# Optimization experiments

Measured on AMD Instinct MI355X. Metric: run time of the kernel, lower is better.

Reference implementation:

```python
import jax, jax.numpy as jnp
import numpy as np

DIM = 2048
NUM_HEADS = 16
HEAD_DIM = DIM // NUM_HEADS  # 128
LC = HEAD_DIM // 2           # 64 complex pairs per head
B, S = 2, 2048
EPS = 1e-6


def setup_inputs() -> dict:
    key = jax.random.key(0)
    ks = jax.random.split(key, 12)
    x = jax.random.normal(ks[0], (B, S, DIM), dtype=jnp.float32)
    # freqs: unit-modulus complex rotations stored as (cos, sin), shape [S,1,LC,2]
    theta = jax.random.uniform(ks[1], (S, 1, LC), dtype=jnp.float32) * (2.0 * np.pi)
    freqs = jnp.stack([jnp.cos(theta), jnp.sin(theta)], axis=-1)
    scale = 0.02
    wq = jax.random.normal(ks[2], (DIM, DIM), dtype=jnp.float32) * scale
    bq = jnp.zeros((DIM,), dtype=jnp.float32)
    wk = jax.random.normal(ks[3], (DIM, DIM), dtype=jnp.float32) * scale
    bk = jnp.zeros((DIM,), dtype=jnp.float32)
    wv = jax.random.normal(ks[4], (DIM, DIM), dtype=jnp.float32) * scale
    bv = jnp.zeros((DIM,), dtype=jnp.float32)
    wo = jax.random.normal(ks[5], (DIM, DIM), dtype=jnp.float32) * scale
    bo = jnp.zeros((DIM,), dtype=jnp.float32)
    gq = jnp.ones((DIM,), dtype=jnp.float32)   # RMSNorm weight for q
    gk = jnp.ones((DIM,), dtype=jnp.float32)   # RMSNorm weight for k
    return {"x": x, "freqs": freqs, "wq": wq, "bq": bq, "wk": wk, "bk": bk,
            "wv": wv, "bv": bv, "wo": wo, "bo": bo, "gq": gq, "gk": gk}


def _rms_norm(x, g):
    xf = x.astype(jnp.float32)
    y = xf * jax.lax.rsqrt(jnp.mean(xf * xf, axis=-1, keepdims=True) + EPS)
    return y.astype(x.dtype) * g


def _rope_apply(x, freqs):
    # x: [B,S,D] -> complex pairs [B,S,H,LC,2]; freqs: [S,1,LC,2] (cos,sin)
    b, s, _ = x.shape
    xp = x.astype(jnp.float32).reshape(b, s, NUM_HEADS, LC, 2)
    xr, xi = xp[..., 0], xp[..., 1]
    cr = freqs[None, :, :, :, 0]  # [1,S,1,LC]
    ci = freqs[None, :, :, :, 1]
    out_r = xr * cr - xi * ci
    out_i = xr * ci + xi * cr
    out = jnp.stack([out_r, out_i], axis=-1).reshape(b, s, DIM)
    return out.astype(x.dtype)


def _attention(q, k, v):
    # q,k,v: [B,S,D] -> multihead SDPA -> [B,S,D]
    b, s, _ = q.shape
    qh = q.reshape(b, s, NUM_HEADS, HEAD_DIM).transpose(0, 2, 1, 3)
    kh = k.reshape(b, s, NUM_HEADS, HEAD_DIM).transpose(0, 2, 1, 3)
    vh = v.reshape(b, s, NUM_HEADS, HEAD_DIM).transpose(0, 2, 1, 3)
    scale = 1.0 / np.sqrt(HEAD_DIM).astype(np.float32)
    scores = jnp.einsum('bhqd,bhkd->bhqk', qh, kh) * scale
    probs = jax.nn.softmax(scores, axis=-1)
    out = jnp.einsum('bhqk,bhkd->bhqd', probs, vh)
    return out.transpose(0, 2, 1, 3).reshape(b, s, DIM)


def reference(x, freqs, wq, bq, wk, bk, wv, bv, wo, bo, gq, gk):
    q = _rms_norm(x @ wq.T + bq, gq)
    k = _rms_norm(x @ wk.T + bk, gk)
    v = x @ wv.T + bv
    q = _rope_apply(q, freqs)
    k = _rope_apply(k, freqs)
    attn = _attention(q, k, v)
    return attn @ wo.T + bo
```

## Files before the change

kernel.cpp:

```cpp
#include <hip/hip_runtime.h>
#include <cstdint>

typedef __bf16 bf16;
typedef __bf16 bf16x8 __attribute__((ext_vector_type(8)));
typedef __bf16 bf16x4 __attribute__((ext_vector_type(4)));
typedef float f32x4 __attribute__((ext_vector_type(4)));

#define DIMN 2048
#define SEQ  2048
#define NH   16
#define HD   128

__device__ __forceinline__ void gld_lds16(const bf16* g, bf16* l) {
    __builtin_amdgcn_global_load_lds(
        (const __attribute__((address_space(1))) void*)g,
        (__attribute__((address_space(3))) void*)l,
        16, 0, 0);
}

__global__ __launch_bounds__(256) void cast_all(
    const float* __restrict__ x,
    const float* __restrict__ wq, const float* __restrict__ wk,
    const float* __restrict__ wv, const float* __restrict__ wo,
    bf16* __restrict__ xb,
    bf16* __restrict__ wqb, bf16* __restrict__ wkb,
    bf16* __restrict__ wvb, bf16* __restrict__ wob)
{
    int id = blockIdx.x;
    const float* src; bf16* dst; int i;
    if (id < 8192) { src = x; dst = xb; i = id * 256 + threadIdx.x; }
    else {
        id -= 8192;
        int w = id >> 12; id &= 4095;
        src = (w == 0) ? wq : (w == 1) ? wk : (w == 2) ? wv : wo;
        dst = (w == 0) ? wqb : (w == 1) ? wkb : (w == 2) ? wvb : wob;
        i = id * 256 + threadIdx.x;
    }
    float4 v = ((const float4*)src)[i];
    bf16x4 o;
    o[0] = (bf16)v.x; o[1] = (bf16)v.y; o[2] = (bf16)v.z; o[3] = (bf16)v.w;
    ((bf16x4*)dst)[i] = o;
}

template<int OUT_F32>
__global__ __launch_bounds__(256) void gemm_bt(
    const bf16* __restrict__ A,
    const bf16* __restrict__ Bw0, const bf16* __restrict__ Bw1, const bf16* __restrict__ Bw2,
    const float* __restrict__ bias0, const float* __restrict__ bias1, const float* __restrict__ bias2,
    void* __restrict__ C0, void* __restrict__ C1, void* __restrict__ C2)
{
    const int K = DIMN, N = DIMN;
    const int vtm = (!OUT_F32) && (blockIdx.z == 2);
    const bf16* Ap; const bf16* Bp; const float* bias; void* Cout;
    if (blockIdx.z == 0)      { Ap = A;   Bp = Bw0; bias = bias0; Cout = C0; }
    else if (blockIdx.z == 1) { Ap = A;   Bp = Bw1; bias = bias1; Cout = C1; }
    else                      { Ap = Bw2; Bp = A;   bias = bias2; Cout = C2; }

    __shared__ __attribute__((aligned(16))) bf16 As[128 * 64];
    __shared__ __attribute__((aligned(16))) bf16 Bs[128 * 64];

    const int t    = threadIdx.x;
    const int lane = t & 63, wave = t >> 6;
    const int l15  = lane & 15, quad = lane >> 4;
    const int wm   = (wave >> 1) * 64, wn = (wave & 1) * 64;
    const long bm = vtm ? (long)blockIdx.x * 128 : (long)blockIdx.y * 128;
    const long bn = vtm ? (long)blockIdx.y * 128 : (long)blockIdx.x * 128;

    const bf16* agp[4]; const bf16* bgp[4]; bf16* asd[4]; bf16* bsd[4];
#pragma unroll
    for (int it = 0; it < 4; it++) {
        int fs  = it * 256 + t;
        int row = fs >> 3;
        int gs  = (fs & 7) ^ (row & 7);
        agp[it] = Ap + (bm + row) * (long)K + gs * 8;
        bgp[it] = Bp + (bn + row) * (long)K + gs * 8;
        asd[it] = As + fs * 8;
        bsd[it] = Bs + fs * 8;
    }
    const int swl = l15 & 7;

    f32x4 acc[4][4] = {};

    for (int k0 = 0; k0 < K; k0 += 64) {
#pragma unroll
        for (int it = 0; it < 4; it++) {
            gld_lds16(agp[it] + k0, asd[it]);
            gld_lds16(bgp[it] + k0, bsd[it]);
        }
        __syncthreads();

#pragma unroll
        for (int ks2 = 0; ks2 < 2; ks2++) {
            const int sw = ((ks2 * 4 + quad) ^ swl) * 8;
            bf16x8 af[4], bfr[4];
#pragma unroll
            for (int i = 0; i < 4; i++)
                af[i] = *(const bf16x8*)(As + (wm + i * 16 + l15) * 64 + sw);
#pragma unroll
            for (int j = 0; j < 4; j++)
                bfr[j] = *(const bf16x8*)(Bs + (wn + j * 16 + l15) * 64 + sw);
#pragma unroll
            for (int i = 0; i < 4; i++)
#pragma unroll
                for (int j = 0; j < 4; j++)
                    acc[i][j] = __builtin_amdgcn_mfma_f32_16x16x32_bf16(af[i], bfr[j], acc[i][j], 0, 0, 0);
        }
        __syncthreads();
    }

    if (vtm) {
#pragma unroll
        for (int j = 0; j < 4; j++) {
            const long col = bn + wn + j * 16 + l15;
            const long cb = col >> 11, cs = col & (SEQ - 1);
#pragma unroll
            for (int i = 0; i < 4; i++) {
                const long m0 = bm + wm + i * 16 + quad * 4;
#pragma unroll
                for (int r = 0; r < 4; r++)
                    ((bf16*)Cout)[((cb * DIMN + m0 + r) * SEQ) + cs] =
                        (bf16)(acc[i][j][r] + bias[m0 + r]);
            }
        }
    } else {
#pragma unroll
        for (int j = 0; j < 4; j++) {
            const long col = bn + wn + j * 16 + l15;
            const float bv = bias[col];
#pragma unroll
            for (int i = 0; i < 4; i++) {
                const long row0 = bm + wm + i * 16 + quad * 4;
#pragma unroll
                for (int r = 0; r < 4; r++) {
                    float v = acc[i][j][r] + bv;
                    if (OUT_F32) ((float*)Cout)[(row0 + r) * N + col] = v;
                    else         ((bf16*)Cout)[(row0 + r) * N + col] = (bf16)v;
                }
            }
        }
    }
}

__global__ __launch_bounds__(256) void norm_prep(
    bf16* __restrict__ q, bf16* __restrict__ k,
    const float* __restrict__ gq, const float* __restrict__ gk,
    const float* __restrict__ freqs)
{
    const int id = blockIdx.x;
    const int t = threadIdx.x;
    const int qk  = id >> 12;
    const int row = id & 4095;
    bf16* ptr = qk ? k : q;
    const float* g = qk ? gk : gq;
    const float osc = qk ? 1.0f : 0.12753138080219222f;
    const int s = row & (SEQ - 1);
    const int lane = t & 63, wave = t >> 6;

    bf16* base = ptr + (long)row * DIMN + t * 8;
    bf16x8 raw = *(const bf16x8*)base;
    float v[8]; float ss = 0.f;
#pragma unroll
    for (int j = 0; j < 8; j++) { v[j] = (float)raw[j]; ss += v[j] * v[j]; }
#pragma unroll
    for (int off = 32; off; off >>= 1) ss += __shfl_xor(ss, off, 64);
    __shared__ float red[4];
    if (lane == 0) red[wave] = ss;
    __syncthreads();
    float tot = red[0] + red[1] + red[2] + red[3];
    float rn = rsqrtf(tot * (1.0f / DIMN) + 1e-6f);

    const int e0 = t * 8;
    bf16x8 o;
#pragma unroll
    for (int pp = 0; pp < 4; pp++) {
        int e = e0 + pp * 2;
        float xr = v[pp * 2]     * rn * g[e];
        float xi = v[pp * 2 + 1] * rn * g[e + 1];
        int lc = (e >> 1) & 63;
        float cr = freqs[s * 128 + lc * 2];
        float ci = freqs[s * 128 + lc * 2 + 1];
        o[pp * 2]     = (bf16)((xr * cr - xi * ci) * osc);
        o[pp * 2 + 1] = (bf16)((xr * ci + xi * cr) * osc);
    }
    *(bf16x8*)base = o;
}

__global__ __launch_bounds__(512, 2) void attention(
    const bf16* __restrict__ Q, const bf16* __restrict__ Kb,
    const bf16* __restrict__ Vt, bf16* __restrict__ O)
{
    __shared__ __attribute__((aligned(16))) bf16 Ksh[2][64 * 128];
    __shared__ __attribute__((aligned(16))) bf16 Vsh[2][128 * 64];
    __shared__ __attribute__((aligned(16))) bf16 Psh[8][32 * 72];
    __shared__ float Lsh[8][32];

    const int t = threadIdx.x;
    const int lane = t & 63, w = t >> 6;
    const int l15 = lane & 15, quad = lane >> 4;
    const int bh = blockIdx.x, b = bh >> 4, h = bh & 15;
    const int qt = blockIdx.y;
    const long qrow0 = (long)b * SEQ + qt * 256 + w * 32;
    const bf16* qbase = Q  + qrow0 * DIMN + h * HD;
    const bf16* kbase = Kb + (long)b * SEQ * DIMN + h * HD;
    const bf16* vbase = Vt + (long)bh * HD * SEQ;

    bf16x8 qf[2][4];
#pragma unroll
    for (int im = 0; im < 2; im++)
#pragma unroll
        for (int kd = 0; kd < 4; kd++)
            qf[im][kd] = *(const bf16x8*)(qbase + (long)(im * 16 + l15) * DIMN + kd * 32 + quad * 8);

    long koff[2], voff[2];
#pragma unroll
    for (int it = 0; it < 2; it++) {
        int fs = it * 512 + t;
        int kr = fs >> 4, kp = fs & 15;
        koff[it] = (long)kr * DIMN + (kp ^ (kr & 15)) * 8;
        int dr = fs >> 3, vp = fs & 7;
        voff[it] = (long)dr * SEQ + (vp ^ (dr & 7)) * 8;
    }

    f32x4 o_acc[2][8] = {};
    float Lt[2] = {0.f, 0.f};

#pragma unroll
    for (int it = 0; it < 2; it++) {
        gld_lds16(kbase + koff[it], &Ksh[0][(it * 512 + t) * 8]);
        gld_lds16(vbase + voff[it], &Vsh[0][(it * 512 + t) * 8]);
    }
    __syncthreads();

    for (int kt = 0; kt < 32; kt++) {
        const int cur = kt & 1;
        if (kt < 31) {
            const bf16* kg = kbase + (long)((kt + 1) * 64) * DIMN;
            const bf16* vg = vbase + (kt + 1) * 64;
#pragma unroll
            for (int it = 0; it < 2; it++) {
                gld_lds16(kg + koff[it], &Ksh[cur ^ 1][(it * 512 + t) * 8]);
                gld_lds16(vg + voff[it], &Vsh[cur ^ 1][(it * 512 + t) * 8]);
            }
        }
        const bf16* K0 = Ksh[cur];
        const bf16* V0 = Vsh[cur];

        f32x4 st[4][2] = {};
        __builtin_amdgcn_s_setprio(1);
#pragma unroll
        for (int jk = 0; jk < 4; jk++)
#pragma unroll
            for (int kd = 0; kd < 4; kd++) {
                bf16x8 kf = *(const bf16x8*)(K0 + (jk * 16 + l15) * 128 + (((kd * 4 + quad) ^ l15) & 15) * 8);
                st[jk][0] = __builtin_amdgcn_mfma_f32_16x16x32_bf16(kf, qf[0][kd], st[jk][0], 0, 0, 0);
                st[jk][1] = __builtin_amdgcn_mfma_f32_16x16x32_bf16(kf, qf[1][kd], st[jk][1], 0, 0, 0);
            }
        __builtin_amdgcn_s_setprio(0);

#pragma unroll
        for (int im = 0; im < 2; im++) {
            float part = 0.f;
#pragma unroll
            for (int jk = 0; jk < 4; jk++) {
                bf16x4 pk;
#pragma unroll
                for (int r = 0; r < 4; r++) {
                    float e = exp2f(st[jk][im][r]);
                    part += e;
                    pk[r] = (bf16)e;
                }
                *(bf16x4*)(Psh[w] + (im * 16 + l15) * 72 + jk * 16 + quad * 4) = pk;
            }
            Lt[im] += part;
        }

        __builtin_amdgcn_s_setprio(1);
#pragma unroll
        for (int kd2 = 0; kd2 < 2; kd2++) {
            bf16x8 pa[2];
            pa[0] = *(const bf16x8*)(Psh[w] + (l15)      * 72 + kd2 * 32 + quad * 8);
            pa[1] = *(const bf16x8*)(Psh[w] + (16 + l15) * 72 + kd2 * 32 + quad * 8);
#pragma unroll
            for (int dj = 0; dj < 8; dj++) {
                bf16x8 vfr = *(const bf16x8*)(V0 + (dj * 16 + l15) * 64 + (((kd2 * 4 + quad) ^ l15) & 7) * 8);
                o_acc[0][dj] = __builtin_amdgcn_mfma_f32_16x16x32_bf16(pa[0], vfr, o_acc[0][dj], 0, 0, 0);
                o_acc[1][dj] = __builtin_amdgcn_mfma_f32_16x16x32_bf16(pa[1], vfr, o_acc[1][dj], 0, 0, 0);
            }
        }
        __builtin_amdgcn_s_setprio(0);
        __syncthreads();
    }

#pragma unroll
    for (int im = 0; im < 2; im++) {
        Lt[im] += __shfl_xor(Lt[im], 16, 64);
        Lt[im] += __shfl_xor(Lt[im], 32, 64);
    }
    if (quad == 0) { Lsh[w][l15] = Lt[0]; Lsh[w][16 + l15] = Lt[1]; }
    __syncthreads();

#pragma unroll
    for (int im = 0; im < 2; im++)
#pragma unroll
        for (int r = 0; r < 4; r++) {
            float inv = 1.0f / Lsh[w][im * 16 + quad * 4 + r];
            long orow = qrow0 + im * 16 + quad * 4 + r;
#pragma unroll
            for (int dj = 0; dj < 8; dj++)
                O[orow * DIMN + h * HD + dj * 16 + l15] = (bf16)(o_acc[im][dj][r] * inv);
        }
}

extern "C" void kernel_launch(void* const* d_in, const int* in_sizes, int n_in,
                              void* d_out, int out_size, void* d_ws, size_t ws_size,
                              hipStream_t stream) {
    const float* x     = (const float*)d_in[0];
    const float* freqs = (const float*)d_in[1];
    const float* wq    = (const float*)d_in[2];
    const float* bq    = (const float*)d_in[3];
    const float* wk    = (const float*)d_in[4];
    const float* bk    = (const float*)d_in[5];
    const float* wv    = (const float*)d_in[6];
    const float* bv    = (const float*)d_in[7];
    const float* wo    = (const float*)d_in[8];
    const float* bo    = (const float*)d_in[9];
    const float* gq    = (const float*)d_in[10];
    const float* gk    = (const float*)d_in[11];
    float* out = (float*)d_out;

    const size_t MAT  = (size_t)4096 * 2048 * 2;
    const size_t WMAT = (size_t)2048 * 2048 * 2;
    char* p = (char*)d_ws;
    bf16* xb  = (bf16*)p; p += MAT;
    bf16* wqb = (bf16*)p; p += WMAT;
    bf16* wkb = (bf16*)p; p += WMAT;
    bf16* wvb = (bf16*)p; p += WMAT;
    bf16* wob = (bf16*)p; p += WMAT;
    bf16* qb  = (bf16*)p; p += MAT;
    bf16* kb  = (bf16*)p; p += MAT;
    bf16* vt  = (bf16*)p; p += MAT;
    bf16* attn = qb;

    cast_all<<<24576, 256, 0, stream>>>(x, wq, wk, wv, wo, xb, wqb, wkb, wvb, wob);

    gemm_bt<0><<<dim3(16, 32, 3), 256, 0, stream>>>(xb, wqb, wkb, wvb,
                                                    bq, bk, bv, qb, kb, vt);

    norm_prep<<<8192, 256, 0, stream>>>(qb, kb, gq, gk, freqs);
    attention<<<dim3(32, 8), 512, 0, stream>>>(qb, kb, vt, attn);
    gemm_bt<1><<<dim3(16, 32, 1), 256, 0, stream>>>(attn, wob, wob, wob,
                                                    bo, bo, bo, out, out, out);
}
```

Before: 401.9 us.

## Replace QKV projection GEMM with 256x256 double-buffered pipelined kernel

Adds a new gemm256 kernel for the fused Q/K/V projection. It uses 256x256 tiles with 8 waves, double-buffered LDS, and staggered async global-to-LDS loads interleaved with MFMA phases under explicit vmcnt waits and s_setprio. It also remaps blocks through a swizzle for better L2 locality. The aim is more data reuse per tile and overlap of memory loads with compute, at the cost of 128KB LDS per block, high register pressure and a fragile hand-tuned wait schedule. The old gemm_bt is simplified to the non-transposed path and is still used for the output projection.

```diff
diff --git a/kernel.cpp b/kernel.cpp
--- a/kernel.cpp
+++ b/kernel.cpp
@@ -50,11 +50,9 @@
     void* __restrict__ C0, void* __restrict__ C1, void* __restrict__ C2)
 {
     const int K = DIMN, N = DIMN;
-    const int vtm = (!OUT_F32) && (blockIdx.z == 2);
-    const bf16* Ap; const bf16* Bp; const float* bias; void* Cout;
-    if (blockIdx.z == 0)      { Ap = A;   Bp = Bw0; bias = bias0; Cout = C0; }
-    else if (blockIdx.z == 1) { Ap = A;   Bp = Bw1; bias = bias1; Cout = C1; }
-    else                      { Ap = Bw2; Bp = A;   bias = bias2; Cout = C2; }
+    const bf16* Bw = Bw0; const float* bias = bias0; void* Cout = C0;
+    if (blockIdx.z == 1) { Bw = Bw1; bias = bias1; Cout = C1; }
+    if (blockIdx.z == 2) { Bw = Bw2; bias = bias2; Cout = C2; }
 
     __shared__ __attribute__((aligned(16))) bf16 As[128 * 64];
     __shared__ __attribute__((aligned(16))) bf16 Bs[128 * 64];
@@ -63,8 +61,8 @@
     const int lane = t & 63, wave = t >> 6;
     const int l15  = lane & 15, quad = lane >> 4;
     const int wm   = (wave >> 1) * 64, wn = (wave & 1) * 64;
-    const long bm = vtm ? (long)blockIdx.x * 128 : (long)blockIdx.y * 128;
-    const long bn = vtm ? (long)blockIdx.y * 128 : (long)blockIdx.x * 128;
+    const long bm  = (long)blockIdx.y * 128;
+    const long bn  = (long)blockIdx.x * 128;
 
     const bf16* agp[4]; const bf16* bgp[4]; bf16* asd[4]; bf16* bsd[4];
 #pragma unroll
@@ -72,8 +70,8 @@
         int fs  = it * 256 + t;
         int row = fs >> 3;
         int gs  = (fs & 7) ^ (row & 7);
-        agp[it] = Ap + (bm + row) * (long)K + gs * 8;
-        bgp[it] = Bp + (bn + row) * (long)K + gs * 8;
+        agp[it] = A  + (bm + row) * (long)K + gs * 8;
+        bgp[it] = Bw + (bn + row) * (long)K + gs * 8;
         asd[it] = As + fs * 8;
         bsd[it] = Bs + fs * 8;
     }
@@ -108,34 +106,152 @@
         __syncthreads();
     }
 
+#pragma unroll
+    for (int j = 0; j < 4; j++) {
+        const long col = bn + wn + j * 16 + l15;
+        const float bv = bias[col];
+#pragma unroll
+        for (int i = 0; i < 4; i++) {
+            const long row0 = bm + wm + i * 16 + quad * 4;
+#pragma unroll
+            for (int r = 0; r < 4; r++) {
+                float v = acc[i][j][r] + bv;
+                if (OUT_F32) ((float*)Cout)[(row0 + r) * N + col] = v;
+                else         ((bf16*)Cout)[(row0 + r) * N + col] = (bf16)v;
+            }
+        }
+    }
+}
+
+#define VMCNT(n) asm volatile("s_waitcnt vmcnt(" #n ")" ::: "memory")
+
+#define STAGE_AQ(bsel, kt, q) do {                                            \
+    const int row_ = (q) * 32 + arow_base;                                    \
+    gld_lds16(Ag + (long)row_ * DIMN + (kt) * 64 + ((ssg ^ (row_ & 7)) << 3), \
+              &As[bsel][(row_ * 8 + ssg) * 8]);                               \
+} while (0)
+
+#define STAGE_BU(bsel, kt, u) do {                                            \
+    const int row_ = (u) * 64 + srl;                                          \
+    gld_lds16(Bg + (long)row_ * DIMN + (kt) * 64 + ((ssg ^ (row_ & 7)) << 3), \
+              &Bs[bsel][(row_ * 8 + ssg) * 8]);                               \
+} while (0)
+
+#define PHASE(bsel, p0, STAGES, WAIT) do {                                    \
+    bf16x8 af_[2][2];                                                         \
+    _Pragma("unroll")                                                         \
+    for (int im = 0; im < 2; ++im) {                                          \
+        const int ar = wm * 128 + ((p0) * 2 + im) * 16 + l15;                 \
+        _Pragma("unroll")                                                     \
+        for (int ks = 0; ks < 2; ++ks)                                        \
+            af_[im][ks] = *(const bf16x8*)(&As[bsel][(ar * 8 + ((ks * 4 + quad) ^ swl)) * 8]); \
+    }                                                                         \
+    if ((p0) == 0) {                                                          \
+        _Pragma("unroll")                                                     \
+        for (int j = 0; j < 4; ++j) {                                         \
+            const int br = wn * 64 + j * 16 + l15;                            \
+            _Pragma("unroll")                                                 \
+            for (int ks = 0; ks < 2; ++ks)                                    \
+                bfrag[j][ks] = *(const bf16x8*)(&Bs[bsel][(br * 8 + ((ks * 4 + quad) ^ swl)) * 8]); \
+        }                                                                     \
+    }                                                                         \
+    STAGES;                                                                   \
+    __builtin_amdgcn_s_setprio(1);                                            \
+    _Pragma("unroll")                                                         \
+    for (int im = 0; im < 2; ++im)                                            \
+        _Pragma("unroll")                                                     \
+        for (int j = 0; j < 4; ++j)                                           \
+            _Pragma("unroll")                                                 \
+            for (int ks = 0; ks < 2; ++ks)                                    \
+                acc[(p0) * 2 + im][j] = __builtin_amdgcn_mfma_f32_16x16x32_bf16( \
+                    af_[im][ks], bfrag[j][ks], acc[(p0) * 2 + im][j], 0, 0, 0); \
+    __builtin_amdgcn_s_setprio(0);                                            \
+    WAIT;                                                                     \
+    asm volatile("" ::: "memory");                                            \
+    __builtin_amdgcn_s_barrier();                                             \
+    asm volatile("" ::: "memory");                                            \
+} while (0)
+
+__global__ __launch_bounds__(512, 2) void gemm256(
+    const bf16* __restrict__ A,
+    const bf16* __restrict__ Bw0, const bf16* __restrict__ Bw1, const bf16* __restrict__ Bw2,
+    const float* __restrict__ bias0, const float* __restrict__ bias1, const float* __restrict__ bias2,
+    bf16* __restrict__ C0, bf16* __restrict__ C1, bf16* __restrict__ C2)
+{
+    const int vtm = (blockIdx.z == 2);
+    const bf16* Ap; const bf16* Bp; const float* bias; bf16* Cout;
+    if (blockIdx.z == 0)      { Ap = A;   Bp = Bw0; bias = bias0; Cout = C0; }
+    else if (blockIdx.z == 1) { Ap = A;   Bp = Bw1; bias = bias1; Cout = C1; }
+    else                      { Ap = Bw2; Bp = A;   bias = bias2; Cout = C2; }
+
+    __shared__ __attribute__((aligned(16))) bf16 As[2][256 * 64];
+    __shared__ __attribute__((aligned(16))) bf16 Bs[2][256 * 64];
+
+    const int t    = threadIdx.x;
+    const int lane = t & 63, wave = t >> 6;
+    const int l15  = lane & 15, quad = lane >> 4;
+    const int wm   = wave >> 2, wn = wave & 3;
+    const int swl  = l15 & 7;
+
+    const int id  = blockIdx.y * 8 + blockIdx.x;
+    const int wg  = (id & 7) * 16 + (id >> 3);
+    const long bm_n = (long)(wg >> 3) * 256;
+    const long bn_n = (long)(wg & 7) * 256;
+    const long bm = vtm ? bn_n : bm_n;
+    const long bn = vtm ? bm_n : bn_n;
+
+    const bf16* Ag = Ap + bm * DIMN;
+    const bf16* Bg = Bp + bn * DIMN;
+
+    const int srl = t >> 3, ssg = t & 7;
+    const int arow_base = (srl & 31) + ((srl >> 5) << 7);
+
+    f32x4  acc[8][4] = {};
+    bf16x8 bfrag[4][2];
+
+    STAGE_BU(0, 0, 0); STAGE_BU(0, 0, 1); STAGE_BU(0, 0, 2); STAGE_BU(0, 0, 3);
+    STAGE_AQ(0, 0, 0); STAGE_AQ(0, 0, 1); STAGE_AQ(0, 0, 2); STAGE_AQ(0, 0, 3);
+    STAGE_BU(1, 1, 0); STAGE_BU(1, 1, 1); STAGE_BU(1, 1, 2); STAGE_BU(1, 1, 3);
+    VMCNT(7);
+    asm volatile("" ::: "memory");
+    __builtin_amdgcn_s_barrier();
+    asm volatile("" ::: "memory");
+
+    for (int kt = 0; kt < 32; ++kt) {
+        const int buf = kt & 1;
+        const int tp1 = (kt + 1) & 31;
+        const int tp2 = (kt + 2) & 31;
+        PHASE(buf, 0, { STAGE_AQ(buf ^ 1, tp1, 0); STAGE_AQ(buf ^ 1, tp1, 1); }, VMCNT(8));
+        PHASE(buf, 1, { STAGE_AQ(buf ^ 1, tp1, 2); STAGE_AQ(buf ^ 1, tp1, 3); }, VMCNT(9));
+        PHASE(buf, 2, { STAGE_BU(buf,     tp2, 0); STAGE_BU(buf,     tp2, 1); }, VMCNT(8));
+        PHASE(buf, 3, { STAGE_BU(buf,     tp2, 2); STAGE_BU(buf,     tp2, 3); }, VMCNT(7));
+    }
+
     if (vtm) {
 #pragma unroll
-        for (int j = 0; j < 4; j++) {
-            const long col = bn + wn + j * 16 + l15;
+        for (int j = 0; j < 4; ++j) {
+            const long col = bn + wn * 64 + j * 16 + l15;
             const long cb = col >> 11, cs = col & (SEQ - 1);
 #pragma unroll
-            for (int i = 0; i < 4; i++) {
-                const long m0 = bm + wm + i * 16 + quad * 4;
-#pragma unroll
-                for (int r = 0; r < 4; r++)
-                    ((bf16*)Cout)[((cb * DIMN + m0 + r) * SEQ) + cs] =
+            for (int i = 0; i < 8; ++i) {
+                const long m0 = bm + wm * 128 + i * 16 + quad * 4;
+#pragma unroll
+                for (int r = 0; r < 4; ++r)
+                    Cout[((cb * DIMN + m0 + r) * SEQ) + cs] =
                         (bf16)(acc[i][j][r] + bias[m0 + r]);
             }
         }
     } else {
 #pragma unroll
-        for (int j = 0; j < 4; j++) {
-            const long col = bn + wn + j * 16 + l15;
+        for (int j = 0; j < 4; ++j) {
+            const long col = bn + wn * 64 + j * 16 + l15;
             const float bv = bias[col];
 #pragma unroll
-            for (int i = 0; i < 4; i++) {
-                const long row0 = bm + wm + i * 16 + quad * 4;
-#pragma unroll
-                for (int r = 0; r < 4; r++) {
-                    float v = acc[i][j][r] + bv;
-                    if (OUT_F32) ((float*)Cout)[(row0 + r) * N + col] = v;
-                    else         ((bf16*)Cout)[(row0 + r) * N + col] = (bf16)v;
-                }
+            for (int i = 0; i < 8; ++i) {
+                const long row0 = bm + wm * 128 + i * 16 + quad * 4;
+#pragma unroll
+                for (int r = 0; r < 4; ++r)
+                    Cout[(row0 + r) * DIMN + col] = (bf16)(acc[i][j][r] + bv);
             }
         }
     }
@@ -343,8 +459,8 @@
 
     cast_all<<<24576, 256, 0, stream>>>(x, wq, wk, wv, wo, xb, wqb, wkb, wvb, wob);
 
-    gemm_bt<0><<<dim3(16, 32, 3), 256, 0, stream>>>(xb, wqb, wkb, wvb,
-                                                    bq, bk, bv, qb, kb, vt);
+    gemm256<<<dim3(8, 16, 3), 512, 0, stream>>>(xb, wqb, wkb, wvb,
+                                                bq, bk, bv, qb, kb, vt);
 
     norm_prep<<<8192, 256, 0, stream>>>(qb, kb, gq, gk, freqs);
     attention<<<dim3(32, 8), 512, 0, stream>>>(qb, kb, vt, attn);
```

Result: slower. 448.3 us (+11.5%).

## Halve attention q-tile per wave and pass P via bpermute instead of LDS

Applied to the files above, without the earlier changes.

Each wave now handles 16 query rows instead of 32, the grid doubles along the query axis, and launch bounds ask for 4 blocks per CU. The probability tile no longer goes through an LDS round-trip. It is packed with v_cvt_pk_bf16_f32 and redistributed into the MFMA A-operand layout with ds_bpermute, and the final row-sum normalisation uses shuffles instead of shared memory. This cuts per-thread registers and LDS use to raise occupancy. In exchange, K/V tiles get half as much reuse per block, so L2/HBM traffic for K and V doubles.

```diff
diff --git a/kernel.cpp b/kernel.cpp
--- a/kernel.cpp
+++ b/kernel.cpp
@@ -185,31 +185,28 @@
     *(bf16x8*)base = o;
 }
 
-__global__ __launch_bounds__(512, 2) void attention(
+__global__ __launch_bounds__(512, 4) void attention(
     const bf16* __restrict__ Q, const bf16* __restrict__ Kb,
     const bf16* __restrict__ Vt, bf16* __restrict__ O)
 {
     __shared__ __attribute__((aligned(16))) bf16 Ksh[2][64 * 128];
     __shared__ __attribute__((aligned(16))) bf16 Vsh[2][128 * 64];
-    __shared__ __attribute__((aligned(16))) bf16 Psh[8][32 * 72];
-    __shared__ float Lsh[8][32];
 
     const int t = threadIdx.x;
     const int lane = t & 63, w = t >> 6;
     const int l15 = lane & 15, quad = lane >> 4;
+    const int hi = quad >> 1;
     const int bh = blockIdx.x, b = bh >> 4, h = bh & 15;
     const int qt = blockIdx.y;
-    const long qrow0 = (long)b * SEQ + qt * 256 + w * 32;
+    const long qrow0 = (long)b * SEQ + qt * 128 + w * 16;
     const bf16* qbase = Q  + qrow0 * DIMN + h * HD;
     const bf16* kbase = Kb + (long)b * SEQ * DIMN + h * HD;
     const bf16* vbase = Vt + (long)bh * HD * SEQ;
 
-    bf16x8 qf[2][4];
-#pragma unroll
-    for (int im = 0; im < 2; im++)
-#pragma unroll
-        for (int kd = 0; kd < 4; kd++)
-            qf[im][kd] = *(const bf16x8*)(qbase + (long)(im * 16 + l15) * DIMN + kd * 32 + quad * 8);
+    bf16x8 qf[4];
+#pragma unroll
+    for (int kd = 0; kd < 4; kd++)
+        qf[kd] = *(const bf16x8*)(qbase + (long)l15 * DIMN + kd * 32 + quad * 8);
 
     long koff[2], voff[2];
 #pragma unroll
@@ -221,8 +218,11 @@
         voff[it] = (long)dr * SEQ + (vp ^ (dr & 7)) * 8;
     }
 
-    f32x4 o_acc[2][8] = {};
-    float Lt[2] = {0.f, 0.f};
+    const int srcA = (((quad & 1) * 2) * 16 + l15) * 4;
+    const int srcB = srcA + 64;
+
+    f32x4 o_acc[8] = {};
+    float Lt = 0.f;
 
 #pragma unroll
     for (int it = 0; it < 2; it++) {
@@ -245,70 +245,70 @@
         const bf16* K0 = Ksh[cur];
         const bf16* V0 = Vsh[cur];
 
-        f32x4 st[4][2] = {};
+        f32x4 st[4] = {};
         __builtin_amdgcn_s_setprio(1);
 #pragma unroll
         for (int jk = 0; jk < 4; jk++)
 #pragma unroll
             for (int kd = 0; kd < 4; kd++) {
                 bf16x8 kf = *(const bf16x8*)(K0 + (jk * 16 + l15) * 128 + (((kd * 4 + quad) ^ l15) & 15) * 8);
-                st[jk][0] = __builtin_amdgcn_mfma_f32_16x16x32_bf16(kf, qf[0][kd], st[jk][0], 0, 0, 0);
-                st[jk][1] = __builtin_amdgcn_mfma_f32_16x16x32_bf16(kf, qf[1][kd], st[jk][1], 0, 0, 0);
+                st[jk] = __builtin_amdgcn_mfma_f32_16x16x32_bf16(kf, qf[kd], st[jk], 0, 0, 0);
             }
         __builtin_amdgcn_s_setprio(0);
 
-#pragma unroll
-        for (int im = 0; im < 2; im++) {
-            float part = 0.f;
-#pragma unroll
-            for (int jk = 0; jk < 4; jk++) {
-                bf16x4 pk;
-#pragma unroll
-                for (int r = 0; r < 4; r++) {
-                    float e = exp2f(st[jk][im][r]);
-                    part += e;
-                    pk[r] = (bf16)e;
-                }
-                *(bf16x4*)(Psh[w] + (im * 16 + l15) * 72 + jk * 16 + quad * 4) = pk;
-            }
-            Lt[im] += part;
+        uint32_t pk0[4], pk1[4];
+#pragma unroll
+        for (int jk = 0; jk < 4; jk++) {
+            float e0 = exp2f(st[jk][0]);
+            float e1 = exp2f(st[jk][1]);
+            float e2 = exp2f(st[jk][2]);
+            float e3 = exp2f(st[jk][3]);
+            Lt += (e0 + e1) + (e2 + e3);
+            uint32_t lo, hiw;
+            asm("v_cvt_pk_bf16_f32 %0, %1, %2" : "=v"(lo)  : "v"(e0), "v"(e1));
+            asm("v_cvt_pk_bf16_f32 %0, %1, %2" : "=v"(hiw) : "v"(e2), "v"(e3));
+            pk0[jk] = lo; pk1[jk] = hiw;
         }
 
         __builtin_amdgcn_s_setprio(1);
 #pragma unroll
         for (int kd2 = 0; kd2 < 2; kd2++) {
-            bf16x8 pa[2];
-            pa[0] = *(const bf16x8*)(Psh[w] + (l15)      * 72 + kd2 * 32 + quad * 8);
-            pa[1] = *(const bf16x8*)(Psh[w] + (16 + l15) * 72 + kd2 * 32 + quad * 8);
+            int a0 = __builtin_amdgcn_ds_bpermute(srcA, (int)pk0[kd2 * 2]);
+            int a1 = __builtin_amdgcn_ds_bpermute(srcA, (int)pk0[kd2 * 2 + 1]);
+            int b0 = __builtin_amdgcn_ds_bpermute(srcA, (int)pk1[kd2 * 2]);
+            int b1 = __builtin_amdgcn_ds_bpermute(srcA, (int)pk1[kd2 * 2 + 1]);
+            int c0 = __builtin_amdgcn_ds_bpermute(srcB, (int)pk0[kd2 * 2]);
+            int c1 = __builtin_amdgcn_ds_bpermute(srcB, (int)pk0[kd2 * 2 + 1]);
+            int d0 = __builtin_amdgcn_ds_bpermute(srcB, (int)pk1[kd2 * 2]);
+            int d1 = __builtin_amdgcn_ds_bpermute(srcB, (int)pk1[kd2 * 2 + 1]);
+            union { uint32_t u[4]; bf16x8 v; } pu;
+            pu.u[0] = hi ? (uint32_t)a1 : (uint32_t)a0;
+            pu.u[1] = hi ? (uint32_t)b1 : (uint32_t)b0;
+            pu.u[2] = hi ? (uint32_t)c1 : (uint32_t)c0;
+            pu.u[3] = hi ? (uint32_t)d1 : (uint32_t)d0;
+            bf16x8 pa = pu.v;
 #pragma unroll
             for (int dj = 0; dj < 8; dj++) {
                 bf16x8 vfr = *(const bf16x8*)(V0 + (dj * 16 + l15) * 64 + (((kd2 * 4 + quad) ^ l15) & 7) * 8);
-                o_acc[0][dj] = __builtin_amdgcn_mfma_f32_16x16x32_bf16(pa[0], vfr, o_acc[0][dj], 0, 0, 0);
-                o_acc[1][dj] = __builtin_amdgcn_mfma_f32_16x16x32_bf16(pa[1], vfr, o_acc[1][dj], 0, 0, 0);
+                o_acc[dj] = __builtin_amdgcn_mfma_f32_16x16x32_bf16(pa, vfr, o_acc[dj], 0, 0, 0);
             }
         }
         __builtin_amdgcn_s_setprio(0);
         __syncthreads();
     }
 
-#pragma unroll
-    for (int im = 0; im < 2; im++) {
-        Lt[im] += __shfl_xor(Lt[im], 16, 64);
-        Lt[im] += __shfl_xor(Lt[im], 32, 64);
-    }
-    if (quad == 0) { Lsh[w][l15] = Lt[0]; Lsh[w][16 + l15] = Lt[1]; }
-    __syncthreads();
-
-#pragma unroll
-    for (int im = 0; im < 2; im++)
-#pragma unroll
-        for (int r = 0; r < 4; r++) {
-            float inv = 1.0f / Lsh[w][im * 16 + quad * 4 + r];
-            long orow = qrow0 + im * 16 + quad * 4 + r;
-#pragma unroll
-            for (int dj = 0; dj < 8; dj++)
-                O[orow * DIMN + h * HD + dj * 16 + l15] = (bf16)(o_acc[im][dj][r] * inv);
-        }
+    Lt += __shfl_xor(Lt, 16, 64);
+    Lt += __shfl_xor(Lt, 32, 64);
+
+#pragma unroll
+    for (int r = 0; r < 4; r++) {
+        float Lr = __shfl(Lt, quad * 4 + r, 64);
+        float inv = 1.0f / Lr;
+        long orow = qrow0 + quad * 4 + r;
+#pragma unroll
+        for (int dj = 0; dj < 8; dj++)
+            O[orow * DIMN + h * HD + dj * 16 + l15] = (bf16)(o_acc[dj][r] * inv);
+    }
 }
 
 extern "C" void kernel_launch(void* const* d_in, const int* in_sizes, int n_in,
@@ -347,7 +347,7 @@
                                                     bq, bk, bv, qb, kb, vt);
 
     norm_prep<<<8192, 256, 0, stream>>>(qb, kb, gq, gk, freqs);
-    attention<<<dim3(32, 8), 512, 0, stream>>>(qb, kb, vt, attn);
+    attention<<<dim3(32, 16), 512, 0, stream>>>(qb, kb, vt, attn);
     gemm_bt<1><<<dim3(16, 32, 1), 256, 0, stream>>>(attn, wob, wob, wob,
                                                     bo, bo, bo, out, out, out);
 }
```

Result: no change. 400.6 us (-0.3%).

## Pass softmax probabilities via ds_bpermute and shrink attention blocks to four waves

Applied to the files above, without the earlier changes.

The P matrix no longer round-trips through shared memory. Each wave now repacks its exp2 scores with v_cvt_pk_bf16_f32 and reshuffles them into MFMA A-operand layout with ds_bpermute. The row-sum reduction for normalization uses a shuffle instead of an LDS table plus a block barrier. The attention block shrinks from 512 to 256 threads (128 query rows) with twice as many blocks, so each K/V tile in LDS is shared by fewer waves and global loads per tile double per thread.

```diff
diff --git a/kernel.cpp b/kernel.cpp
--- a/kernel.cpp
+++ b/kernel.cpp
@@ -185,21 +185,20 @@
     *(bf16x8*)base = o;
 }
 
-__global__ __launch_bounds__(512, 2) void attention(
+__global__ __launch_bounds__(256, 2) void attention(
     const bf16* __restrict__ Q, const bf16* __restrict__ Kb,
     const bf16* __restrict__ Vt, bf16* __restrict__ O)
 {
     __shared__ __attribute__((aligned(16))) bf16 Ksh[2][64 * 128];
     __shared__ __attribute__((aligned(16))) bf16 Vsh[2][128 * 64];
-    __shared__ __attribute__((aligned(16))) bf16 Psh[8][32 * 72];
-    __shared__ float Lsh[8][32];
 
     const int t = threadIdx.x;
     const int lane = t & 63, w = t >> 6;
     const int l15 = lane & 15, quad = lane >> 4;
+    const int hi = quad >> 1;
     const int bh = blockIdx.x, b = bh >> 4, h = bh & 15;
     const int qt = blockIdx.y;
-    const long qrow0 = (long)b * SEQ + qt * 256 + w * 32;
+    const long qrow0 = (long)b * SEQ + qt * 128 + w * 32;
     const bf16* qbase = Q  + qrow0 * DIMN + h * HD;
     const bf16* kbase = Kb + (long)b * SEQ * DIMN + h * HD;
     const bf16* vbase = Vt + (long)bh * HD * SEQ;
@@ -211,23 +210,26 @@
         for (int kd = 0; kd < 4; kd++)
             qf[im][kd] = *(const bf16x8*)(qbase + (long)(im * 16 + l15) * DIMN + kd * 32 + quad * 8);
 
-    long koff[2], voff[2];
-#pragma unroll
-    for (int it = 0; it < 2; it++) {
-        int fs = it * 512 + t;
+    long koff[4], voff[4];
+#pragma unroll
+    for (int it = 0; it < 4; it++) {
+        int fs = it * 256 + t;
         int kr = fs >> 4, kp = fs & 15;
         koff[it] = (long)kr * DIMN + (kp ^ (kr & 15)) * 8;
         int dr = fs >> 3, vp = fs & 7;
         voff[it] = (long)dr * SEQ + (vp ^ (dr & 7)) * 8;
     }
 
+    const int srcA = (((quad & 1) * 2) * 16 + l15) * 4;
+    const int srcB = srcA + 64;
+
     f32x4 o_acc[2][8] = {};
     float Lt[2] = {0.f, 0.f};
 
 #pragma unroll
-    for (int it = 0; it < 2; it++) {
-        gld_lds16(kbase + koff[it], &Ksh[0][(it * 512 + t) * 8]);
-        gld_lds16(vbase + voff[it], &Vsh[0][(it * 512 + t) * 8]);
+    for (int it = 0; it < 4; it++) {
+        gld_lds16(kbase + koff[it], &Ksh[0][(it * 256 + t) * 8]);
+        gld_lds16(vbase + voff[it], &Vsh[0][(it * 256 + t) * 8]);
     }
     __syncthreads();
 
@@ -237,9 +239,9 @@
             const bf16* kg = kbase + (long)((kt + 1) * 64) * DIMN;
             const bf16* vg = vbase + (kt + 1) * 64;
 #pragma unroll
-            for (int it = 0; it < 2; it++) {
-                gld_lds16(kg + koff[it], &Ksh[cur ^ 1][(it * 512 + t) * 8]);
-                gld_lds16(vg + voff[it], &Vsh[cur ^ 1][(it * 512 + t) * 8]);
+            for (int it = 0; it < 4; it++) {
+                gld_lds16(kg + koff[it], &Ksh[cur ^ 1][(it * 256 + t) * 8]);
+                gld_lds16(vg + voff[it], &Vsh[cur ^ 1][(it * 256 + t) * 8]);
             }
         }
         const bf16* K0 = Ksh[cur];
@@ -257,29 +259,43 @@
             }
         __builtin_amdgcn_s_setprio(0);
 
-#pragma unroll
-        for (int im = 0; im < 2; im++) {
-            float part = 0.f;
+        uint32_t pk0[2][4], pk1[2][4];
+#pragma unroll
+        for (int im = 0; im < 2; im++)
 #pragma unroll
             for (int jk = 0; jk < 4; jk++) {
-                bf16x4 pk;
-#pragma unroll
-                for (int r = 0; r < 4; r++) {
-                    float e = exp2f(st[jk][im][r]);
-                    part += e;
-                    pk[r] = (bf16)e;
-                }
-                *(bf16x4*)(Psh[w] + (im * 16 + l15) * 72 + jk * 16 + quad * 4) = pk;
-            }
-            Lt[im] += part;
-        }
+                float e0 = exp2f(st[jk][im][0]);
+                float e1 = exp2f(st[jk][im][1]);
+                float e2 = exp2f(st[jk][im][2]);
+                float e3 = exp2f(st[jk][im][3]);
+                Lt[im] += (e0 + e1) + (e2 + e3);
+                uint32_t lo, hiw;
+                asm("v_cvt_pk_bf16_f32 %0, %1, %2" : "=v"(lo)  : "v"(e0), "v"(e1));
+                asm("v_cvt_pk_bf16_f32 %0, %1, %2" : "=v"(hiw) : "v"(e2), "v"(e3));
+                pk0[im][jk] = lo; pk1[im][jk] = hiw;
+            }
 
         __builtin_amdgcn_s_setprio(1);
 #pragma unroll
         for (int kd2 = 0; kd2 < 2; kd2++) {
             bf16x8 pa[2];
-            pa[0] = *(const bf16x8*)(Psh[w] + (l15)      * 72 + kd2 * 32 + quad * 8);
-            pa[1] = *(const bf16x8*)(Psh[w] + (16 + l15) * 72 + kd2 * 32 + quad * 8);
+#pragma unroll
+            for (int im = 0; im < 2; im++) {
+                int a0 = __builtin_amdgcn_ds_bpermute(srcA, (int)pk0[im][kd2 * 2]);
+                int a1 = __builtin_amdgcn_ds_bpermute(srcA, (int)pk0[im][kd2 * 2 + 1]);
+                int b0 = __builtin_amdgcn_ds_bpermute(srcA, (int)pk1[im][kd2 * 2]);
+                int b1 = __builtin_amdgcn_ds_bpermute(srcA, (int)pk1[im][kd2 * 2 + 1]);
+                int c0 = __builtin_amdgcn_ds_bpermute(srcB, (int)pk0[im][kd2 * 2]);
+                int c1 = __builtin_amdgcn_ds_bpermute(srcB, (int)pk0[im][kd2 * 2 + 1]);
+                int d0 = __builtin_amdgcn_ds_bpermute(srcB, (int)pk1[im][kd2 * 2]);
+                int d1 = __builtin_amdgcn_ds_bpermute(srcB, (int)pk1[im][kd2 * 2 + 1]);
+                union { uint32_t u[4]; bf16x8 v; } pu;
+                pu.u[0] = hi ? (uint32_t)a1 : (uint32_t)a0;
+                pu.u[1] = hi ? (uint32_t)b1 : (uint32_t)b0;
+                pu.u[2] = hi ? (uint32_t)c1 : (uint32_t)c0;
+                pu.u[3] = hi ? (uint32_t)d1 : (uint32_t)d0;
+                pa[im] = pu.v;
+            }
 #pragma unroll
             for (int dj = 0; dj < 8; dj++) {
                 bf16x8 vfr = *(const bf16x8*)(V0 + (dj * 16 + l15) * 64 + (((kd2 * 4 + quad) ^ l15) & 7) * 8);
@@ -296,14 +312,13 @@
         Lt[im] += __shfl_xor(Lt[im], 16, 64);
         Lt[im] += __shfl_xor(Lt[im], 32, 64);
     }
-    if (quad == 0) { Lsh[w][l15] = Lt[0]; Lsh[w][16 + l15] = Lt[1]; }
-    __syncthreads();
 
 #pragma unroll
     for (int im = 0; im < 2; im++)
 #pragma unroll
         for (int r = 0; r < 4; r++) {
-            float inv = 1.0f / Lsh[w][im * 16 + quad * 4 + r];
+            float Lr = __shfl(Lt[im], quad * 4 + r, 64);
+            float inv = 1.0f / Lr;
             long orow = qrow0 + im * 16 + quad * 4 + r;
 #pragma unroll
             for (int dj = 0; dj < 8; dj++)
@@ -347,7 +362,7 @@
                                                     bq, bk, bv, qb, kb, vt);
 
     norm_prep<<<8192, 256, 0, stream>>>(qb, kb, gq, gk, freqs);
-    attention<<<dim3(32, 8), 512, 0, stream>>>(qb, kb, vt, attn);
+    attention<<<dim3(32, 16), 256, 0, stream>>>(qb, kb, vt, attn);
     gemm_bt<1><<<dim3(16, 32, 1), 256, 0, stream>>>(attn, wob, wob, wob,
                                                     bo, bo, bo, out, out, out);
 }
```

Measured after the change: 412.4 us. +2.6%, slower.
